# Optimization experiments

Hardware: AMD Instinct MI355X
Metric: run time of the kernel (lower is better)

## Reference

```python
import jax, jax.numpy as jnp
import numpy as np

B, N, D_IN, D_OUT, NUM_RING = 32, 8192, 64, 128, 4
BN_EPS = 1e-5


def setup_inputs() -> dict:
    key = jax.random.key(0)
    ks = jax.random.split(key, 8)
    return {
        "x": jax.random.normal(ks[0], (B, D_IN, N), dtype=jnp.float32),
        "ring": jax.random.randint(ks[1], (B, N), 0, NUM_RING, dtype=jnp.int64),
        "W": jax.random.normal(ks[2], (NUM_RING, D_OUT, D_IN), dtype=jnp.float32) * 0.1,
        "b": jax.random.normal(ks[3], (NUM_RING, D_OUT), dtype=jnp.float32) * 0.1,
        "gamma": jax.random.uniform(ks[4], (NUM_RING, D_OUT), dtype=jnp.float32) + 0.5,
        "beta": jax.random.normal(ks[5], (NUM_RING, D_OUT), dtype=jnp.float32) * 0.1,
        "mean": jax.random.normal(ks[6], (NUM_RING, D_OUT), dtype=jnp.float32) * 0.1,
        "var": jax.random.uniform(ks[7], (NUM_RING, D_OUT), dtype=jnp.float32) + 0.5,
    }


def reference(x, ring, W, b, gamma, beta, mean, var):
    # x: [B, 64, N]; ring: [B, N] int labels in [0, num_ring)
    xt = jnp.transpose(x, (0, 2, 1))  # [B, N, 64]
    Bv, Nv, _ = xt.shape
    num_ring = W.shape[0]
    out = jnp.zeros((Bv, Nv, W.shape[1]), dtype=x.dtype)
    neg = jnp.finfo(x.dtype).min
    for i in range(num_ring):  # small fixed loop over rings
        # 1x1 conv == per-point linear, then BatchNorm (inference-mode affine)
        y = jnp.einsum("bnd,od->bno", xt, W[i]) + b[i]  # [B, N, 128]
        scale = gamma[i] * jax.lax.rsqrt(var[i] + BN_EPS)
        y = (y - mean[i]) * scale + beta[i]
        m = (ring == i)[..., None]  # [B, N, 1]
        # per-(batch, ring) segment max over points, broadcast back to members
        ymax = jnp.max(jnp.where(m, y, neg), axis=1, keepdims=True)  # [B, 1, 128]
        out = jnp.where(m, ymax, out)
    return jnp.transpose(out, (0, 2, 1))  # [B, 128, N]
```

## Files before the change

### kernel.cpp

```cpp
#include <hip/hip_runtime.h>
#include <hip/hip_bf16.h>
#include <cstdint>
#include <cstddef>

#define BB 32
#define NN 8192
#define DIN 64
#define DOUT 128
#define NR 4
#define BN_EPS 1e-5f

typedef float nfloat4 __attribute__((ext_vector_type(4)));
typedef float floatx4 __attribute__((ext_vector_type(4)));
typedef short short8 __attribute__((ext_vector_type(8)));


__device__ inline void pack2(float a, float b, short8& dst, int idx) {
  __hip_bfloat162 h = __float22bfloat162_rn(make_float2(a, b));
  const unsigned int bits = *(unsigned int*)&h;
  dst[idx] = (short)(bits & 0xffffu);
  dst[idx + 1] = (short)(bits >> 16);
}

__global__ void __launch_bounds__(256) k_compute(
    const float* __restrict__ x, const float* __restrict__ W,
    const int* __restrict__ ring, unsigned int* __restrict__ smax_keys) {
  const int b = blockIdx.y;
  const int n0 = blockIdx.x * 256;
  const int wave = (int)threadIdx.x >> 6;
  const int lane = (int)threadIdx.x & 63;
  const int quad = lane >> 4;
  const int l16 = lane & 15;
  const float* xb = x + (size_t)b * DIN * NN;
  const int* rgb = ring + (size_t)b * NN;

  short8 afr[NR][2][2];
#pragma unroll
  for (int r = 0; r < NR; ++r) {
#pragma unroll
    for (int tt = 0; tt < 2; ++tt) {
      const int chan = (wave + 4 * tt) * 16 + l16;
      const float* wr = W + ((size_t)r * DOUT + chan) * DIN + quad * 8;
#pragma unroll
      for (int ks = 0; ks < 2; ++ks) {
        const float4 w0 = *(const float4*)&wr[ks * 32];
        const float4 w1 = *(const float4*)&wr[ks * 32 + 4];
        short8 a;
        pack2(w0.x, w0.y, a, 0);
        pack2(w0.z, w0.w, a, 2);
        pack2(w1.x, w1.y, a, 4);
        pack2(w1.z, w1.w, a, 6);
        afr[r][tt][ks] = a;
      }
    }
  }

  floatx4 rmax[2][NR];
#pragma unroll
  for (int tt = 0; tt < 2; ++tt)
#pragma unroll
    for (int r = 0; r < NR; ++r)
      rmax[tt][r] = {-INFINITY, -INFINITY, -INFINITY, -INFINITY};

  float bx[16];
  int rn;
  auto LD = [&](int T) {
    const int n = n0 + T * 16 + l16;
#pragma unroll
    for (int j = 0; j < 8; ++j) {
      bx[j] = xb[(size_t)(quad * 8 + j) * NN + n];
      bx[8 + j] = xb[(size_t)(32 + quad * 8 + j) * NN + n];
    }
    rn = rgb[n];
  };

  LD(0);
#pragma unroll 1
  for (int T = 0; T < 16; ++T) {
    short8 b0, b1;
#pragma unroll
    for (int j = 0; j < 4; ++j) {
      pack2(bx[2 * j], bx[2 * j + 1], b0, 2 * j);
      pack2(bx[8 + 2 * j], bx[8 + 2 * j + 1], b1, 2 * j);
    }
    const int rr = rn;
    if (T < 15) LD(T + 1);

#pragma unroll
    for (int r = 0; r < NR; ++r) {
      floatx4 acc0 = {0.f, 0.f, 0.f, 0.f};
      floatx4 acc1 = {0.f, 0.f, 0.f, 0.f};
      acc0 = __builtin_amdgcn_mfma_f32_16x16x32_bf16(afr[r][0][0], b0, acc0, 0, 0, 0);
      acc0 = __builtin_amdgcn_mfma_f32_16x16x32_bf16(afr[r][0][1], b1, acc0, 0, 0, 0);
      acc1 = __builtin_amdgcn_mfma_f32_16x16x32_bf16(afr[r][1][0], b0, acc1, 0, 0, 0);
      acc1 = __builtin_amdgcn_mfma_f32_16x16x32_bf16(afr[r][1][1], b1, acc1, 0, 0, 0);
      const bool m = (rr == r);
#pragma unroll
      for (int p = 0; p < 4; ++p) {
        rmax[0][r][p] = fmaxf(rmax[0][r][p], m ? acc0[p] : -INFINITY);
        rmax[1][r][p] = fmaxf(rmax[1][r][p], m ? acc1[p] : -INFINITY);
      }
    }
  }

#pragma unroll
  for (int tt = 0; tt < 2; ++tt) {
#pragma unroll
    for (int r = 0; r < NR; ++r) {
#pragma unroll
      for (int p = 0; p < 4; ++p) {
        float v = rmax[tt][r][p];
        v = fmaxf(v, __shfl_xor(v, 1, 64));
        v = fmaxf(v, __shfl_xor(v, 2, 64));
        v = fmaxf(v, __shfl_xor(v, 4, 64));
        v = fmaxf(v, __shfl_xor(v, 8, 64));
        if (l16 == 0) {
          const int chan = (wave + 4 * tt) * 16 + quad * 4 + p;
          const unsigned int u = __float_as_uint(v);
          const unsigned int key = (u & 0x80000000u) ? ~u : (u | 0x80000000u);
          atomicMax(&smax_keys[(size_t)(b * NR + r) * DOUT + chan], key);
        }
      }
    }
  }
}

__global__ void __launch_bounds__(256) k_out(
    const float* __restrict__ bias, const float* __restrict__ gamma,
    const float* __restrict__ beta, const float* __restrict__ mean,
    const float* __restrict__ var, const int* __restrict__ ring,
    const unsigned int* __restrict__ smax_keys, float* __restrict__ out) {
  const int b = blockIdx.z;
  const int og = blockIdx.y;
  const int n0 = blockIdx.x * 1024;
  const int t = (int)threadIdx.x;

  __shared__ float lut[32 * NR * 32];
  {
    const int oo = t >> 3;
    const int r = (t >> 1) & 3;
    const int c0 = (t & 1) * 16;
    const int o = og * 32 + oo;
    const int tt = r * DOUT + o;
    const unsigned int key = smax_keys[(size_t)b * NR * DOUT + tt];
    const unsigned int u = (key & 0x80000000u) ? (key ^ 0x80000000u) : ~key;
    const float raw = __uint_as_float(u);
    const float sc = gamma[tt] * rsqrtf(var[tt] + BN_EPS);
    const float val = (raw + bias[tt] - mean[tt]) * sc + beta[tt];
    nfloat4 v4 = {val, val, val, val};
    float* dst = &lut[(oo * NR + r) * 32 + c0];
#pragma unroll
    for (int k = 0; k < 4; ++k) *(nfloat4*)&dst[k * 4] = v4;
  }
  __syncthreads();

  const int n = n0 + t * 4;
  const int4 rg = *(const int4*)&ring[(size_t)b * NN + n];
  const int l31 = t & 31;
  const float* p0 = &lut[rg.x * 32 + l31];
  const float* p1 = &lut[rg.y * 32 + l31];
  const float* p2 = &lut[rg.z * 32 + l31];
  const float* p3 = &lut[rg.w * 32 + l31];
  float* orow = out + ((size_t)b * DOUT + og * 32) * NN + n;

#pragma unroll 8
  for (int oo = 0; oo < 32; ++oo) {
    nfloat4 v;
    v.x = p0[oo * 128];
    v.y = p1[oo * 128];
    v.z = p2[oo * 128];
    v.w = p3[oo * 128];
    __builtin_nontemporal_store(v, (nfloat4*)(orow + (size_t)oo * NN));
  }
}

extern "C" void kernel_launch(void* const* d_in, const int* in_sizes, int n_in,
                              void* d_out, int out_size, void* d_ws, size_t ws_size,
                              hipStream_t stream) {
  const float* x = (const float*)d_in[0];
  const int* ring = (const int*)d_in[1];
  const float* W = (const float*)d_in[2];
  const float* bias = (const float*)d_in[3];
  const float* gamma = (const float*)d_in[4];
  const float* beta = (const float*)d_in[5];
  const float* mean = (const float*)d_in[6];
  const float* var = (const float*)d_in[7];
  float* out = (float*)d_out;

  unsigned int* keys = (unsigned int*)d_ws;

  (void)hipMemsetAsync(keys, 0, (size_t)BB * NR * DOUT * 4, stream);

  k_compute<<<dim3(NN / 256, BB), 256, 0, stream>>>(x, W, ring, keys);
  k_out<<<dim3(NN / 1024, DOUT / 32, BB), 256, 0, stream>>>(bias, gamma, beta, mean,
                                                            var, ring, keys, out);
}
```

Before: 230.3 us.

## Stage x tile in LDS with coalesced loads and use register-select output writes

The compute kernel now loads the x tile with coalesced float4 reads, converts it to bf16, and stores it in a swizzled LDS buffer, then reads MFMA operands from LDS. This replaces strided scalar global loads that were software-pipelined through registers. The output kernel drops the shared LUT in favour of one block per output channel that computes the four ring values in registers and selects among them per point. The cost is added LDS use and a barrier in the compute kernel, and the output kernel now reads the ring array once per channel instead of once per group of 32 channels.

Result: no change. 228.2 us (-0.9%).

```diff
diff --git a/kernel.cpp b/kernel.cpp
--- a/kernel.cpp
+++ b/kernel.cpp
@@ -21,6 +21,8 @@
   dst[idx] = (short)(bits & 0xffffu);
   dst[idx + 1] = (short)(bits >> 16);
 }
+
+__device__ inline int swz(int n) { return (n ^ (n >> 2) ^ (n >> 5)) & 7; }
 
 __global__ void __launch_bounds__(256) k_compute(
     const float* __restrict__ x, const float* __restrict__ W,
@@ -34,6 +36,29 @@
   const float* xb = x + (size_t)b * DIN * NN;
   const int* rgb = ring + (size_t)b * NN;
 
+  __shared__ short8 lx[256 * 8];
+
+  {
+    const float* xr = xb + (size_t)(wave * 16) * NN + n0 + 4 * lane;
+#pragma unroll
+    for (int grp = 0; grp < 2; ++grp) {
+      nfloat4 L[8];
+#pragma unroll
+      for (int j = 0; j < 8; ++j)
+        L[j] = *(const nfloat4*)&xr[(size_t)(grp * 8 + j) * NN];
+#pragma unroll
+      for (int i = 0; i < 4; ++i) {
+        short8 v;
+        pack2(L[0][i], L[1][i], v, 0);
+        pack2(L[2][i], L[3][i], v, 2);
+        pack2(L[4][i], L[5][i], v, 4);
+        pack2(L[6][i], L[7][i], v, 6);
+        const int ni = 4 * lane + i;
+        lx[ni * 8 + ((wave * 2 + grp) ^ swz(ni))] = v;
+      }
+    }
+  }
+
   short8 afr[NR][2][2];
 #pragma unroll
   for (int r = 0; r < NR; ++r) {
@@ -62,30 +87,14 @@
     for (int r = 0; r < NR; ++r)
       rmax[tt][r] = {-INFINITY, -INFINITY, -INFINITY, -INFINITY};
 
-  float bx[16];
-  int rn;
-  auto LD = [&](int T) {
-    const int n = n0 + T * 16 + l16;
-#pragma unroll
-    for (int j = 0; j < 8; ++j) {
-      bx[j] = xb[(size_t)(quad * 8 + j) * NN + n];
-      bx[8 + j] = xb[(size_t)(32 + quad * 8 + j) * NN + n];
-    }
-    rn = rgb[n];
-  };
-
-  LD(0);
-#pragma unroll 1
+  __syncthreads();
+
+#pragma unroll 4
   for (int T = 0; T < 16; ++T) {
-    short8 b0, b1;
-#pragma unroll
-    for (int j = 0; j < 4; ++j) {
-      pack2(bx[2 * j], bx[2 * j + 1], b0, 2 * j);
-      pack2(bx[8 + 2 * j], bx[8 + 2 * j + 1], b1, 2 * j);
-    }
-    const int rr = rn;
-    if (T < 15) LD(T + 1);
-
+    const int n = T * 16 + l16;
+    const short8 b0 = lx[n * 8 + (quad ^ swz(n))];
+    const short8 b1 = lx[n * 8 + ((4 + quad) ^ swz(n))];
+    const int rr = rgb[n0 + n];
 #pragma unroll
     for (int r = 0; r < NR; ++r) {
       floatx4 acc0 = {0.f, 0.f, 0.f, 0.f};
@@ -131,47 +140,46 @@
     const float* __restrict__ var, const int* __restrict__ ring,
     const unsigned int* __restrict__ smax_keys, float* __restrict__ out) {
   const int b = blockIdx.z;
-  const int og = blockIdx.y;
-  const int n0 = blockIdx.x * 1024;
+  const int o = blockIdx.y;
+  const int nh = blockIdx.x;
   const int t = (int)threadIdx.x;
 
-  __shared__ float lut[32 * NR * 32];
-  {
-    const int oo = t >> 3;
-    const int r = (t >> 1) & 3;
-    const int c0 = (t & 1) * 16;
-    const int o = og * 32 + oo;
+  auto fin = [&](int r) -> float {
     const int tt = r * DOUT + o;
     const unsigned int key = smax_keys[(size_t)b * NR * DOUT + tt];
     const unsigned int u = (key & 0x80000000u) ? (key ^ 0x80000000u) : ~key;
     const float raw = __uint_as_float(u);
     const float sc = gamma[tt] * rsqrtf(var[tt] + BN_EPS);
-    const float val = (raw + bias[tt] - mean[tt]) * sc + beta[tt];
-    nfloat4 v4 = {val, val, val, val};
-    float* dst = &lut[(oo * NR + r) * 32 + c0];
-#pragma unroll
-    for (int k = 0; k < 4; ++k) *(nfloat4*)&dst[k * 4] = v4;
-  }
-  __syncthreads();
-
-  const int n = n0 + t * 4;
-  const int4 rg = *(const int4*)&ring[(size_t)b * NN + n];
-  const int l31 = t & 31;
-  const float* p0 = &lut[rg.x * 32 + l31];
-  const float* p1 = &lut[rg.y * 32 + l31];
-  const float* p2 = &lut[rg.z * 32 + l31];
-  const float* p3 = &lut[rg.w * 32 + l31];
-  float* orow = out + ((size_t)b * DOUT + og * 32) * NN + n;
-
-#pragma unroll 8
-  for (int oo = 0; oo < 32; ++oo) {
+    return (raw + bias[tt] - mean[tt]) * sc + beta[tt];
+  };
+  const float yv0 = fin(0), yv1 = fin(1), yv2 = fin(2), yv3 = fin(3);
+
+  const int base = nh * (NN / 2);
+  const int* rgb = ring + (size_t)b * NN + base;
+  float* orow = out + ((size_t)b * DOUT + o) * NN + base;
+
+  int4 rg0 = *(const int4*)&rgb[0 * 1024 + t * 4];
+  int4 rg1 = *(const int4*)&rgb[1 * 1024 + t * 4];
+  int4 rg2 = *(const int4*)&rgb[2 * 1024 + t * 4];
+  int4 rg3 = *(const int4*)&rgb[3 * 1024 + t * 4];
+
+  auto sel = [&](int r) -> float {
+    const float lo = (r & 1) ? yv1 : yv0;
+    const float hi = (r & 1) ? yv3 : yv2;
+    return (r & 2) ? hi : lo;
+  };
+  auto emit = [&](const int4& rg, int it) {
     nfloat4 v;
-    v.x = p0[oo * 128];
-    v.y = p1[oo * 128];
-    v.z = p2[oo * 128];
-    v.w = p3[oo * 128];
-    __builtin_nontemporal_store(v, (nfloat4*)(orow + (size_t)oo * NN));
-  }
+    v.x = sel(rg.x);
+    v.y = sel(rg.y);
+    v.z = sel(rg.z);
+    v.w = sel(rg.w);
+    __builtin_nontemporal_store(v, (nfloat4*)&orow[it * 1024 + t * 4]);
+  };
+  emit(rg0, 0);
+  emit(rg1, 1);
+  emit(rg2, 2);
+  emit(rg3, 3);
 }
 
 extern "C" void kernel_launch(void* const* d_in, const int* in_sizes, int n_in,
@@ -192,6 +200,6 @@
   (void)hipMemsetAsync(keys, 0, (size_t)BB * NR * DOUT * 4, stream);
 
   k_compute<<<dim3(NN / 256, BB), 256, 0, stream>>>(x, W, ring, keys);
-  k_out<<<dim3(NN / 1024, DOUT / 32, BB), 256, 0, stream>>>(bias, gamma, beta, mean,
-                                                            var, ring, keys, out);
-}
+  k_out<<<dim3(2, DOUT, BB), 256, 0, stream>>>(bias, gamma, beta, mean,
+                                               var, ring, keys, out);
+}
```

## Stage x tile in LDS with coalesced vector loads and swizzled bf16 layout

Applied to the files above, without the earlier changes.

The compute kernel now loads each block's 256-point slice of x with coalesced float4 loads. It converts the slice to bf16 once and stores it in a swizzled shared-memory layout. The old path had every lane do strided scalar global loads for each 16-point step. The MFMA loop reads its B fragments from LDS instead. The masked max update becomes a conditional branch. Separately, the output kernel replaces its nontemporal stores with ordinary stores. The gains are better global coalescing and less conversion work, at the cost of 32KB of LDS per block, a barrier, and possible divergence in the branch.

Result: no change. 233.8 us (+1.5%).

```diff
diff --git a/kernel.cpp b/kernel.cpp
--- a/kernel.cpp
+++ b/kernel.cpp
@@ -21,6 +21,8 @@
   dst[idx] = (short)(bits & 0xffffu);
   dst[idx + 1] = (short)(bits >> 16);
 }
+
+__device__ inline int swz(int n) { return (n ^ (n >> 2) ^ (n >> 5)) & 7; }
 
 __global__ void __launch_bounds__(256) k_compute(
     const float* __restrict__ x, const float* __restrict__ W,
@@ -34,6 +36,29 @@
   const float* xb = x + (size_t)b * DIN * NN;
   const int* rgb = ring + (size_t)b * NN;
 
+  __shared__ short8 lx[256 * 8];
+
+  {
+    const float* xr = xb + (size_t)(wave * 16) * NN + n0 + 4 * lane;
+#pragma unroll
+    for (int grp = 0; grp < 2; ++grp) {
+      nfloat4 L[8];
+#pragma unroll
+      for (int j = 0; j < 8; ++j)
+        L[j] = *(const nfloat4*)&xr[(size_t)(grp * 8 + j) * NN];
+#pragma unroll
+      for (int i = 0; i < 4; ++i) {
+        short8 v;
+        pack2(L[0][i], L[1][i], v, 0);
+        pack2(L[2][i], L[3][i], v, 2);
+        pack2(L[4][i], L[5][i], v, 4);
+        pack2(L[6][i], L[7][i], v, 6);
+        const int ni = 4 * lane + i;
+        lx[ni * 8 + ((wave * 2 + grp) ^ swz(ni))] = v;
+      }
+    }
+  }
+
   short8 afr[NR][2][2];
 #pragma unroll
   for (int r = 0; r < NR; ++r) {
@@ -62,30 +87,14 @@
     for (int r = 0; r < NR; ++r)
       rmax[tt][r] = {-INFINITY, -INFINITY, -INFINITY, -INFINITY};
 
-  float bx[16];
-  int rn;
-  auto LD = [&](int T) {
-    const int n = n0 + T * 16 + l16;
-#pragma unroll
-    for (int j = 0; j < 8; ++j) {
-      bx[j] = xb[(size_t)(quad * 8 + j) * NN + n];
-      bx[8 + j] = xb[(size_t)(32 + quad * 8 + j) * NN + n];
-    }
-    rn = rgb[n];
-  };
-
-  LD(0);
-#pragma unroll 1
+  __syncthreads();
+
+#pragma unroll 4
   for (int T = 0; T < 16; ++T) {
-    short8 b0, b1;
-#pragma unroll
-    for (int j = 0; j < 4; ++j) {
-      pack2(bx[2 * j], bx[2 * j + 1], b0, 2 * j);
-      pack2(bx[8 + 2 * j], bx[8 + 2 * j + 1], b1, 2 * j);
-    }
-    const int rr = rn;
-    if (T < 15) LD(T + 1);
-
+    const int n = T * 16 + l16;
+    const short8 b0 = lx[n * 8 + (quad ^ swz(n))];
+    const short8 b1 = lx[n * 8 + ((4 + quad) ^ swz(n))];
+    const int rr = rgb[n0 + n];
 #pragma unroll
     for (int r = 0; r < NR; ++r) {
       floatx4 acc0 = {0.f, 0.f, 0.f, 0.f};
@@ -94,11 +103,12 @@
       acc0 = __builtin_amdgcn_mfma_f32_16x16x32_bf16(afr[r][0][1], b1, acc0, 0, 0, 0);
       acc1 = __builtin_amdgcn_mfma_f32_16x16x32_bf16(afr[r][1][0], b0, acc1, 0, 0, 0);
       acc1 = __builtin_amdgcn_mfma_f32_16x16x32_bf16(afr[r][1][1], b1, acc1, 0, 0, 0);
-      const bool m = (rr == r);
-#pragma unroll
-      for (int p = 0; p < 4; ++p) {
-        rmax[0][r][p] = fmaxf(rmax[0][r][p], m ? acc0[p] : -INFINITY);
-        rmax[1][r][p] = fmaxf(rmax[1][r][p], m ? acc1[p] : -INFINITY);
+      if (rr == r) {
+#pragma unroll
+        for (int p = 0; p < 4; ++p) {
+          rmax[0][r][p] = fmaxf(rmax[0][r][p], acc0[p]);
+          rmax[1][r][p] = fmaxf(rmax[1][r][p], acc1[p]);
+        }
       }
     }
   }
@@ -170,7 +180,7 @@
     v.y = p1[oo * 128];
     v.z = p2[oo * 128];
     v.w = p3[oo * 128];
-    __builtin_nontemporal_store(v, (nfloat4*)(orow + (size_t)oo * NN));
+    *(nfloat4*)(orow + (size_t)oo * NN) = v;
   }
 }
 
```
